# Optimization experiments

Measured on AMD Instinct MI355X. Metric: run time of the kernel, lower is better.

## Reference

```python
import jax, jax.numpy as jnp
import numpy as np

B, T, C = 4, 2048, 768
NH, NKV, HD = 12, 12, 64
RMS_EPS = 1e-6


def rms_norm(x):
    return x * jax.lax.rsqrt(jnp.mean(x * x, axis=-1, keepdims=True) + RMS_EPS)


def apply_rotary_emb(x, cos, sin):
    # x: [B,T,H,D], cos/sin: [T,D/2]
    d2 = x.shape[-1] // 2
    x1, x2 = x[..., :d2], x[..., d2:]
    c = cos[None, :, None, :]
    s = sin[None, :, None, :]
    return jnp.concatenate([x1 * c - x2 * s, x1 * s + x2 * c], axis=-1)


def setup_inputs() -> dict:
    key = jax.random.key(0)
    ks = jax.random.split(key, 10)
    inv_freq = 1.0 / (100000.0 ** (np.arange(0, HD, 2, dtype=np.float32) / HD))  # [HD/2]
    t = np.arange(T, dtype=np.float32)
    freqs = np.outer(t, inv_freq)  # [T, HD/2]
    return {
        "x": jax.random.normal(ks[0], (B, T, C), jnp.float32),
        "ve": jax.random.normal(ks[1], (B, T, C), jnp.float32),
        "cos": jnp.asarray(np.cos(freqs)),
        "sin": jnp.asarray(np.sin(freqs)),
        "Wq": jax.random.normal(ks[2], (C, C), jnp.float32) * (1.0 / np.sqrt(C)),
        "Wk": jax.random.normal(ks[3], (C, C), jnp.float32) * (1.0 / np.sqrt(C)),
        "Wv": jax.random.normal(ks[4], (C, C), jnp.float32) * (1.0 / np.sqrt(C)),
        "Wproj": jax.random.normal(ks[5], (C, C), jnp.float32) * (1.0 / np.sqrt(C)),
        "Wgate": jax.random.normal(ks[6], (NKV, 12), jnp.float32) * 0.1,
        "window_left": 1024,
    }


def reference(x, ve, cos, sin, Wq, Wk, Wv, Wproj, Wgate, window_left):
    q = (x @ Wq.T).reshape(B, T, NH, HD)
    k = (x @ Wk.T).reshape(B, T, NKV, HD)
    v = (x @ Wv.T).reshape(B, T, NKV, HD)

    # value-embedding gating (has_ve path): gate = 3*sigmoid(Linear(x[...,:12]))
    ve_h = ve.reshape(B, T, NKV, HD)
    gate = 3.0 * jax.nn.sigmoid(x[..., :12] @ Wgate.T)  # [B,T,NKV]
    v = v + gate[..., None] * ve_h

    q = apply_rotary_emb(q, cos, sin)
    k = apply_rotary_emb(k, cos, sin)
    q = rms_norm(q) * 1.2
    k = rms_norm(k) * 1.2

    # sliding-window causal bias
    row = jnp.arange(T)[:, None]
    col = jnp.arange(T)[None, :]
    mask = (row >= col) & ((row - col) <= window_left)
    bias = jnp.where(mask, 0.0, -1e9).astype(x.dtype)  # [T,T]

    scale = 1.0 / np.sqrt(HD)
    att = jnp.einsum("bqhd,bkhd->bhqk", q, k) * scale + bias[None, None]
    att = jax.nn.softmax(att, axis=-1)
    y = jnp.einsum("bhqk,bkhd->bqhd", att, v).reshape(B, T, C)
    return y @ Wproj.T
```

## Files before the change

kernel.cpp:

```cpp
#include <hip/hip_runtime.h>
#include <hip/hip_bf16.h>
#include <cstdint>
#include <cstddef>

#define B_  4
#define T_  2048
#define C_  768
#define NH_ 12
#define HD_ 64

typedef __bf16 bf16_t;
typedef __attribute__((ext_vector_type(8))) __bf16 bf16x8;
typedef __attribute__((ext_vector_type(4))) __bf16 bf16x4;
typedef __attribute__((ext_vector_type(4))) float floatx4;
typedef __attribute__((ext_vector_type(8))) unsigned short ushort8;
typedef __attribute__((ext_vector_type(4))) unsigned int uint4v;

#define MFMA16(a, b, c) __builtin_amdgcn_mfma_f32_16x16x32_bf16((a), (b), (c), 0, 0, 0)

#define SM_C1 0.18033688f
#define SM_C2 -17.3123405f

typedef const __attribute__((address_space(1))) uint8_t* gptr_t;
typedef __attribute__((address_space(3))) uint8_t* lptr_t;

static __device__ __forceinline__ void gld16(const void* g, void* l) {
    __builtin_amdgcn_global_load_lds((gptr_t)g, (lptr_t)l, 16, 0, 0);
}

__global__ __launch_bounds__(256) void cvt_all_kernel(
    const void* s0, const void* s1, const void* s2, const void* s3,
    const void* s4, const void* s5, const void* s6, const void* s7, const void* s8,
    bf16_t* d0, bf16_t* d1, bf16_t* d2, bf16_t* d3,
    bf16_t* d4, bf16_t* d5, bf16_t* d6, bf16_t* d7, bf16_t* d8)
{
    const void* srcs[9] = {s0, s1, s2, s3, s4, s5, s6, s7, s8};
    bf16_t*     dsts[9] = {d0, d1, d2, d3, d4, d5, d6, d7, d8};
    const int   ns[9]   = {B_*T_*C_, B_*T_*C_, T_*32, T_*32,
                           C_*C_, C_*C_, C_*C_, C_*C_, 144};
    const int t = blockIdx.y;
    const void* src = srcs[t];
    bf16_t*     dst = dsts[t];
    const int   nc  = ns[t] >> 3;
    const bool isf32 = (((const unsigned short*)s2)[0] == 0);
    const int stride = gridDim.x * 256;
    if (isf32) {
        const float* sf = (const float*)src;
        for (int i = blockIdx.x * 256 + threadIdx.x; i < nc; i += stride) {
            ushort8 o;
#pragma unroll
            for (int j = 0; j < 8; j++) {
                union { float f; unsigned u; } v; v.f = sf[i * 8 + j];
                bf16_t b = (bf16_t)v.f; (void)b;
                o[j] = (unsigned short)(__builtin_bit_cast(unsigned short,
                         (bf16_t)sf[i * 8 + j]));
            }
            *(ushort8*)&dst[i * 8] = o;
        }
    } else {
        const uint4v* sb = (const uint4v*)src;
        uint4v* db = (uint4v*)dst;
        for (int i = blockIdx.x * 256 + threadIdx.x; i < nc; i += stride)
            db[i] = sb[i];
    }
}

template <bool OUT_BF16>
__device__ __forceinline__ void gemm_bt_tile(
    const bf16_t* __restrict__ A, const bf16_t* __restrict__ Bm,
    void* __restrict__ Cout, int m0, int n0, int K, int ldc)
{
    __shared__ bf16_t As[128 * 32];
    __shared__ bf16_t Bs[128 * 32];
    const int tid  = threadIdx.x;
    const int lane = tid & 63;
    const int wid  = tid >> 6;
    const int m16  = lane & 15;
    const int quad = lane >> 4;
    const int wm   = (wid >> 1) * 64;
    const int wn   = (wid & 1) * 64;
    const int srow = lane >> 2;
    const int soct = (lane & 3) * 8;

    floatx4 acc[4][4];
#pragma unroll
    for (int i = 0; i < 4; i++)
#pragma unroll
        for (int j = 0; j < 4; j++) acc[i][j] = (floatx4){0.f, 0.f, 0.f, 0.f};

    for (int k0 = 0; k0 < K; k0 += 32) {
        const bf16_t* ga0 = &A[(size_t)(m0 + 16 * wid + srow) * K + k0 + soct];
        const bf16_t* gb0 = &Bm[(size_t)(n0 + 16 * wid + srow) * K + k0 + soct];
        gld16(ga0,                 (bf16_t*)As + wid * 512);
        gld16(ga0 + (size_t)64 * K, (bf16_t*)As + wid * 512 + 2048);
        gld16(gb0,                 (bf16_t*)Bs + wid * 512);
        gld16(gb0 + (size_t)64 * K, (bf16_t*)Bs + wid * 512 + 2048);
        __syncthreads();
        bf16x8 af[4], bfr[4];
#pragma unroll
        for (int i = 0; i < 4; i++)
            af[i] = *(const bf16x8*)&As[(wm + i * 16 + m16) * 32 + quad * 8];
#pragma unroll
        for (int j = 0; j < 4; j++)
            bfr[j] = *(const bf16x8*)&Bs[(wn + j * 16 + m16) * 32 + quad * 8];
#pragma unroll
        for (int i = 0; i < 4; i++)
#pragma unroll
            for (int j = 0; j < 4; j++)
                acc[i][j] = MFMA16(af[i], bfr[j], acc[i][j]);
        __syncthreads();
    }

#pragma unroll
    for (int i = 0; i < 4; i++) {
#pragma unroll
        for (int j = 0; j < 4; j++) {
            const int colg = n0 + wn + j * 16 + m16;
#pragma unroll
            for (int r = 0; r < 4; r++) {
                const int rowg = m0 + wm + i * 16 + quad * 4 + r;
                if (OUT_BF16)
                    ((bf16_t*)Cout)[(size_t)rowg * ldc + colg] = (bf16_t)acc[i][j][r];
                else
                    ((float*)Cout)[(size_t)rowg * ldc + colg] = acc[i][j][r];
            }
        }
    }
}

__global__ __launch_bounds__(256) void gemm_qkv_kernel(
    const bf16_t* __restrict__ xb,
    const bf16_t* __restrict__ wq, const bf16_t* __restrict__ wk,
    const bf16_t* __restrict__ wv,
    bf16_t* __restrict__ ql, bf16_t* __restrict__ kl, bf16_t* __restrict__ vl)
{
    const int sel = blockIdx.y / 6;
    const int nt  = blockIdx.y % 6;
    const bf16_t* Bm = (sel == 0) ? wq : (sel == 1) ? wk : wv;
    bf16_t* Cout     = (sel == 0) ? ql : (sel == 1) ? kl : vl;
    gemm_bt_tile<true>(xb, Bm, Cout, blockIdx.x * 128, nt * 128, C_, C_);
}

__global__ __launch_bounds__(256) void gemm_proj_kernel(
    const bf16_t* __restrict__ yb, const bf16_t* __restrict__ wp,
    void* __restrict__ out, const void* cos_raw)
{
    const bool isf32 = (((const unsigned short*)cos_raw)[0] == 0);
    if (isf32)
        gemm_bt_tile<false>(yb, wp, out, blockIdx.x * 128, blockIdx.y * 128, C_, C_);
    else
        gemm_bt_tile<true>(yb, wp, out, blockIdx.x * 128, blockIdx.y * 128, C_, C_);
}

__global__ __launch_bounds__(768) void qkv_post_kernel(
    const bf16_t* __restrict__ x, const bf16_t* __restrict__ ve,
    const bf16_t* __restrict__ cosp, const bf16_t* __restrict__ sinp,
    const bf16_t* __restrict__ wg,
    const bf16_t* __restrict__ ql, const bf16_t* __restrict__ kl,
    const bf16_t* __restrict__ vl,
    bf16_t* __restrict__ qb, bf16_t* __restrict__ kb, bf16_t* __restrict__ vt)
{
    const int bt = blockIdx.x;
    const int b  = bt / T_;
    const int t  = bt % T_;
    const int h  = threadIdx.x >> 6;
    const int d  = threadIdx.x & 63;
    const size_t lin    = (size_t)bt * C_ + h * HD_ + d;
    const size_t outIdx = ((size_t)(b * NH_ + h) * T_ + t) * HD_ + d;

    float g = 0.f;
#pragma unroll
    for (int j = 0; j < 12; j++)
        g += (float)x[(size_t)bt * C_ + j] * (float)wg[h * 12 + j];
    const float gate = 3.f / (1.f + __expf(-g));
    const int c6 = t & 63;
    const int tp = (t & ~63) | (((c6 & 15) << 2) | (c6 >> 4));
    vt[((size_t)(b * NH_ + h) * HD_ + d) * T_ + tp] =
        (bf16_t)((float)vl[lin] + gate * (float)ve[lin]);

    const float c = (float)cosp[t * 32 + (d & 31)];
    const float s = (float)sinp[t * 32 + (d & 31)];

    {
        const float own = (float)ql[lin];
        const float oth = __shfl_xor(own, 32, 64);
        const float qr  = (d < 32) ? (own * c - oth * s) : (oth * s + own * c);
        float ss = qr * qr;
#pragma unroll
        for (int off = 1; off < 64; off <<= 1) ss += __shfl_xor(ss, off, 64);
        qb[outIdx] = (bf16_t)(qr * rsqrtf(ss * (1.f / 64.f) + 1e-6f) * 1.2f);
    }
    {
        const float own = (float)kl[lin];
        const float oth = __shfl_xor(own, 32, 64);
        const float kr  = (d < 32) ? (own * c - oth * s) : (oth * s + own * c);
        float ss = kr * kr;
#pragma unroll
        for (int off = 1; off < 64; off <<= 1) ss += __shfl_xor(ss, off, 64);
        kb[outIdx] = (bf16_t)(kr * rsqrtf(ss * (1.f / 64.f) + 1e-6f) * 1.2f);
    }
}

__global__ __launch_bounds__(256, 3) void attn_kernel(
    const bf16_t* __restrict__ Q, const bf16_t* __restrict__ Km,
    const bf16_t* __restrict__ Vtg, bf16_t* __restrict__ Y,
    const int* __restrict__ wl)
{
    const int q0 = blockIdx.x * 128;
    const int bh = blockIdx.y;
    const int b  = bh / NH_;
    const int h  = bh % NH_;
    const int window = wl[0];
    const int tid  = threadIdx.x;
    const int wid  = tid >> 6;
    const int lane = tid & 63;
    const int m16  = lane & 15;
    const int quad = lane >> 4;
    const int qw   = q0 + wid * 32;

    const size_t base = (size_t)bh * T_ * HD_;
    const bf16_t* Qb  = Q + base;
    const bf16_t* Kb  = Km + base;
    const bf16_t* Vb  = Vtg + base;

    __shared__ bf16_t Ks[2][64 * 64];
    __shared__ bf16_t Vs[2][64 * 64];
    __shared__ bf16_t Ps[4][32 * 72];

    bf16x8 qf[2][2];
#pragma unroll
    for (int mt = 0; mt < 2; mt++)
#pragma unroll
        for (int ks = 0; ks < 2; ks++)
            qf[mt][ks] = *(const bf16x8*)
                &Qb[(size_t)(qw + mt * 16 + m16) * HD_ + ks * 32 + quad * 8];

    const int srow = tid >> 2;
    const int soct = tid & 3;
    const int g0   = 2 * soct, g1 = 2 * soct + 1;
    const int kd0  = srow * 64 + ((g0 ^ (srow & 7)) << 3);
    const int kd1  = srow * 64 + ((g1 ^ (srow & 7)) << 3);

    int rsw[2];
#pragma unroll
    for (int ks = 0; ks < 2; ks++)
        rsw[ks] = (((ks * 4 + quad) ^ (m16 & 7)) << 3);

    int lo = q0 - window;
    if (lo < 0) lo = 0;
    lo &= ~63;
    const int nch = (q0 + 128 - lo) >> 6;

    floatx4 accO[2][4];
#pragma unroll
    for (int mt = 0; mt < 2; mt++)
#pragma unroll
        for (int dt = 0; dt < 4; dt++) accO[mt][dt] = (floatx4){0.f, 0.f, 0.f, 0.f};
    float lsum[2][4] = {{0.f, 0.f, 0.f, 0.f}, {0.f, 0.f, 0.f, 0.f}};

    bf16x8 ka0 = *(const bf16x8*)&Kb[(size_t)(lo + srow) * HD_ + g0 * 8];
    bf16x8 ka1 = *(const bf16x8*)&Kb[(size_t)(lo + srow) * HD_ + g1 * 8];
    bf16x8 va0 = *(const bf16x8*)&Vb[(size_t)srow * T_ + lo + g0 * 8];
    bf16x8 va1 = *(const bf16x8*)&Vb[(size_t)srow * T_ + lo + g1 * 8];
    *(bf16x8*)&Ks[0][kd0] = ka0;
    *(bf16x8*)&Ks[0][kd1] = ka1;
    *(bf16x8*)&Vs[0][kd0] = va0;
    *(bf16x8*)&Vs[0][kd1] = va1;

    for (int ic = 0; ic < nch; ic++) {
        const int kc = lo + ic * 64;
        const bool more = (ic + 1 < nch);
        if (more) {
            const int kn = kc + 64;
            ka0 = *(const bf16x8*)&Kb[(size_t)(kn + srow) * HD_ + g0 * 8];
            ka1 = *(const bf16x8*)&Kb[(size_t)(kn + srow) * HD_ + g1 * 8];
            va0 = *(const bf16x8*)&Vb[(size_t)srow * T_ + kn + g0 * 8];
            va1 = *(const bf16x8*)&Vb[(size_t)srow * T_ + kn + g1 * 8];
        }
        __syncthreads();
        const int buf = ic & 1;

        const bool skip = (kc > qw + 31) || (kc + 63 < qw - window);
        if (!skip) {
            bf16x8 kf[4][2];
#pragma unroll
            for (int nt = 0; nt < 4; nt++) {
                const int rb = (nt * 16 + m16) * 64;
                kf[nt][0] = *(const bf16x8*)&Ks[buf][rb + rsw[0]];
                kf[nt][1] = *(const bf16x8*)&Ks[buf][rb + rsw[1]];
            }
            floatx4 sa[2][4];
#pragma unroll
            for (int mt = 0; mt < 2; mt++)
#pragma unroll
                for (int nt = 0; nt < 4; nt++) {
                    floatx4 z = (floatx4){0.f, 0.f, 0.f, 0.f};
                    z = MFMA16(qf[mt][0], kf[nt][0], z);
                    z = MFMA16(qf[mt][1], kf[nt][1], z);
                    sa[mt][nt] = z;
                }

            const bool edge = (kc + 63 > qw) || (kc < qw + 31 - window);
#pragma unroll
            for (int mt = 0; mt < 2; mt++)
#pragma unroll
                for (int r = 0; r < 4; r++) {
                    bf16x4 pk;
                    float psum = 0.f;
                    const int rowg = qw + mt * 16 + quad * 4 + r;
#pragma unroll
                    for (int nt = 0; nt < 4; nt++) {
                        float p = __builtin_amdgcn_exp2f(
                            fmaf(sa[mt][nt][r], SM_C1, SM_C2));
                        if (edge) {
                            const int colg = kc + nt * 16 + m16;
                            const bool ok = (colg <= rowg) &&
                                            (rowg - colg <= window);
                            p = ok ? p : 0.f;
                        }
                        pk[nt] = (bf16_t)p;
                        psum += p;
                    }
                    lsum[mt][r] += psum;
                    *(bf16x4*)&Ps[wid][(mt * 16 + quad * 4 + r) * 72 + m16 * 4] = pk;
                }
            asm volatile("" ::: "memory");

            bf16x8 pa[2][2];
#pragma unroll
            for (int mt = 0; mt < 2; mt++)
#pragma unroll
                for (int ks = 0; ks < 2; ks++)
                    pa[mt][ks] = *(const bf16x8*)
                        &Ps[wid][(mt * 16 + m16) * 72 + ks * 32 + quad * 8];
#pragma unroll
            for (int dt = 0; dt < 4; dt++) {
                const int rb = (dt * 16 + m16) * 64;
                const bf16x8 vf0 = *(const bf16x8*)&Vs[buf][rb + rsw[0]];
                const bf16x8 vf1 = *(const bf16x8*)&Vs[buf][rb + rsw[1]];
#pragma unroll
                for (int mt = 0; mt < 2; mt++) {
                    accO[mt][dt] = MFMA16(pa[mt][0], vf0, accO[mt][dt]);
                    accO[mt][dt] = MFMA16(pa[mt][1], vf1, accO[mt][dt]);
                }
            }
        }

        if (more) {
            const int nb = buf ^ 1;
            *(bf16x8*)&Ks[nb][kd0] = ka0;
            *(bf16x8*)&Ks[nb][kd1] = ka1;
            *(bf16x8*)&Vs[nb][kd0] = va0;
            *(bf16x8*)&Vs[nb][kd1] = va1;
        }
    }

#pragma unroll
    for (int mt = 0; mt < 2; mt++)
#pragma unroll
        for (int r = 0; r < 4; r++) {
            float l = lsum[mt][r];
#pragma unroll
            for (int off = 1; off < 16; off <<= 1) l += __shfl_xor(l, off, 64);
            const float inv = 1.f / l;
            const int tq = qw + mt * 16 + quad * 4 + r;
#pragma unroll
            for (int dt = 0; dt < 4; dt++)
                Y[((size_t)b * T_ + tq) * C_ + h * HD_ + dt * 16 + m16] =
                    (bf16_t)(accO[mt][dt][r] * inv);
        }
}

extern "C" void kernel_launch(void* const* d_in, const int* in_sizes, int n_in,
                              void* d_out, int out_size, void* d_ws, size_t ws_size,
                              hipStream_t stream)
{
    const void* x_raw   = d_in[0];
    const void* ve_raw  = d_in[1];
    const void* cos_raw = d_in[2];
    const void* sin_raw = d_in[3];
    const void* wq_raw  = d_in[4];
    const void* wk_raw  = d_in[5];
    const void* wv_raw  = d_in[6];
    const void* wp_raw  = d_in[7];
    const void* wg_raw  = d_in[8];
    const int*  wl      = (const int*)d_in[9];

    const size_t NTC = (size_t)B_ * T_ * C_;
    const size_t WSZ = (size_t)C_ * C_;

    bf16_t* ws  = (bf16_t*)d_ws;
    bf16_t* xb  = ws;
    bf16_t* veb = xb + NTC;
    bf16_t* cb  = veb + NTC;
    bf16_t* sb  = cb + T_ * 32;
    bf16_t* wqb = sb + T_ * 32;
    bf16_t* wkb = wqb + WSZ;
    bf16_t* wvb = wkb + WSZ;
    bf16_t* wpb = wvb + WSZ;
    bf16_t* wgb = wpb + WSZ;
    bf16_t* ql  = wgb + 256;
    bf16_t* kl  = ql + NTC;
    bf16_t* vl  = kl + NTC;
    bf16_t* qb  = vl + NTC;
    bf16_t* kb  = qb + NTC;
    bf16_t* vt  = kb + NTC;
    bf16_t* yb  = ql;

    cvt_all_kernel<<<dim3(1024, 9), 256, 0, stream>>>(
        x_raw, ve_raw, cos_raw, sin_raw, wq_raw, wk_raw, wv_raw, wp_raw, wg_raw,
        xb, veb, cb, sb, wqb, wkb, wvb, wpb, wgb);

    gemm_qkv_kernel<<<dim3(64, 18), 256, 0, stream>>>(xb, wqb, wkb, wvb, ql, kl, vl);

    qkv_post_kernel<<<dim3(B_ * T_), 768, 0, stream>>>(
        xb, veb, cb, sb, wgb, ql, kl, vl, qb, kb, vt);

    attn_kernel<<<dim3(T_ / 128, B_ * NH_), 256, 0, stream>>>(qb, kb, vt, yb, wl);

    gemm_proj_kernel<<<dim3(64, 6), 256, 0, stream>>>(yb, wpb, d_out, cos_raw);
}
```

Baseline: 270.7 us.

## Keep P in registers, skip masked tiles, stage V transpose, deepen GEMM k-step

Attention now computes S transposed (K as the A operand), so the probability fragments stay in registers and feed the PV MFMA directly without the LDS P buffer. Fully masked 16x16 subtiles are skipped, and query blocks are reordered per head group to balance causal load. qkv_post now handles 32 tokens per wave and transposes V through shared memory so the vt stores coalesce. The GEMM loads two 32-wide K slabs per barrier, halving the number of syncs, and dead code is removed from the convert kernel. The risks are higher register and LDS pressure and extra branch divergence.

```diff
diff --git a/kernel.cpp b/kernel.cpp
--- a/kernel.cpp
+++ b/kernel.cpp
@@ -49,12 +49,9 @@
         for (int i = blockIdx.x * 256 + threadIdx.x; i < nc; i += stride) {
             ushort8 o;
 #pragma unroll
-            for (int j = 0; j < 8; j++) {
-                union { float f; unsigned u; } v; v.f = sf[i * 8 + j];
-                bf16_t b = (bf16_t)v.f; (void)b;
-                o[j] = (unsigned short)(__builtin_bit_cast(unsigned short,
-                         (bf16_t)sf[i * 8 + j]));
-            }
+            for (int j = 0; j < 8; j++)
+                o[j] = (unsigned short)__builtin_bit_cast(unsigned short,
+                         (bf16_t)sf[i * 8 + j]);
             *(ushort8*)&dst[i * 8] = o;
         }
     } else {
@@ -70,8 +67,8 @@
     const bf16_t* __restrict__ A, const bf16_t* __restrict__ Bm,
     void* __restrict__ Cout, int m0, int n0, int K, int ldc)
 {
-    __shared__ bf16_t As[128 * 32];
-    __shared__ bf16_t Bs[128 * 32];
+    __shared__ bf16_t As[2][128 * 32];
+    __shared__ bf16_t Bs[2][128 * 32];
     const int tid  = threadIdx.x;
     const int lane = tid & 63;
     const int wid  = tid >> 6;
@@ -88,26 +85,33 @@
 #pragma unroll
         for (int j = 0; j < 4; j++) acc[i][j] = (floatx4){0.f, 0.f, 0.f, 0.f};
 
-    for (int k0 = 0; k0 < K; k0 += 32) {
+    for (int k0 = 0; k0 < K; k0 += 64) {
         const bf16_t* ga0 = &A[(size_t)(m0 + 16 * wid + srow) * K + k0 + soct];
         const bf16_t* gb0 = &Bm[(size_t)(n0 + 16 * wid + srow) * K + k0 + soct];
-        gld16(ga0,                 (bf16_t*)As + wid * 512);
-        gld16(ga0 + (size_t)64 * K, (bf16_t*)As + wid * 512 + 2048);
-        gld16(gb0,                 (bf16_t*)Bs + wid * 512);
-        gld16(gb0 + (size_t)64 * K, (bf16_t*)Bs + wid * 512 + 2048);
+        gld16(ga0,                       (bf16_t*)As[0] + wid * 512);
+        gld16(ga0 + (size_t)64 * K,      (bf16_t*)As[0] + wid * 512 + 2048);
+        gld16(gb0,                       (bf16_t*)Bs[0] + wid * 512);
+        gld16(gb0 + (size_t)64 * K,      (bf16_t*)Bs[0] + wid * 512 + 2048);
+        gld16(ga0 + 32,                  (bf16_t*)As[1] + wid * 512);
+        gld16(ga0 + (size_t)64 * K + 32, (bf16_t*)As[1] + wid * 512 + 2048);
+        gld16(gb0 + 32,                  (bf16_t*)Bs[1] + wid * 512);
+        gld16(gb0 + (size_t)64 * K + 32, (bf16_t*)Bs[1] + wid * 512 + 2048);
         __syncthreads();
-        bf16x8 af[4], bfr[4];
-#pragma unroll
-        for (int i = 0; i < 4; i++)
-            af[i] = *(const bf16x8*)&As[(wm + i * 16 + m16) * 32 + quad * 8];
-#pragma unroll
-        for (int j = 0; j < 4; j++)
-            bfr[j] = *(const bf16x8*)&Bs[(wn + j * 16 + m16) * 32 + quad * 8];
-#pragma unroll
-        for (int i = 0; i < 4; i++)
+#pragma unroll
+        for (int half = 0; half < 2; half++) {
+            bf16x8 af[4], bfr[4];
+#pragma unroll
+            for (int i = 0; i < 4; i++)
+                af[i] = *(const bf16x8*)&As[half][(wm + i * 16 + m16) * 32 + quad * 8];
 #pragma unroll
             for (int j = 0; j < 4; j++)
-                acc[i][j] = MFMA16(af[i], bfr[j], acc[i][j]);
+                bfr[j] = *(const bf16x8*)&Bs[half][(wn + j * 16 + m16) * 32 + quad * 8];
+#pragma unroll
+            for (int i = 0; i < 4; i++)
+#pragma unroll
+                for (int j = 0; j < 4; j++)
+                    acc[i][j] = MFMA16(af[i], bfr[j], acc[i][j]);
+        }
         __syncthreads();
     }
 
@@ -152,7 +156,7 @@
         gemm_bt_tile<true>(yb, wp, out, blockIdx.x * 128, blockIdx.y * 128, C_, C_);
 }
 
-__global__ __launch_bounds__(768) void qkv_post_kernel(
+__global__ __launch_bounds__(256) void qkv_post_kernel(
     const bf16_t* __restrict__ x, const bf16_t* __restrict__ ve,
     const bf16_t* __restrict__ cosp, const bf16_t* __restrict__ sinp,
     const bf16_t* __restrict__ wg,
@@ -160,44 +164,57 @@
     const bf16_t* __restrict__ vl,
     bf16_t* __restrict__ qb, bf16_t* __restrict__ kb, bf16_t* __restrict__ vt)
 {
-    const int bt = blockIdx.x;
-    const int b  = bt / T_;
-    const int t  = bt % T_;
-    const int h  = threadIdx.x >> 6;
+    const int t0 = blockIdx.x * 32;
+    const int b  = blockIdx.y;
+    const int w  = threadIdx.x >> 6;
+    const int h  = blockIdx.z * 4 + w;
     const int d  = threadIdx.x & 63;
-    const size_t lin    = (size_t)bt * C_ + h * HD_ + d;
-    const size_t outIdx = ((size_t)(b * NH_ + h) * T_ + t) * HD_ + d;
-
-    float g = 0.f;
-#pragma unroll
-    for (int j = 0; j < 12; j++)
-        g += (float)x[(size_t)bt * C_ + j] * (float)wg[h * 12 + j];
-    const float gate = 3.f / (1.f + __expf(-g));
-    const int c6 = t & 63;
-    const int tp = (t & ~63) | (((c6 & 15) << 2) | (c6 >> 4));
-    vt[((size_t)(b * NH_ + h) * HD_ + d) * T_ + tp] =
-        (bf16_t)((float)vl[lin] + gate * (float)ve[lin]);
-
-    const float c = (float)cosp[t * 32 + (d & 31)];
-    const float s = (float)sinp[t * 32 + (d & 31)];
-
-    {
-        const float own = (float)ql[lin];
-        const float oth = __shfl_xor(own, 32, 64);
-        const float qr  = (d < 32) ? (own * c - oth * s) : (oth * s + own * c);
-        float ss = qr * qr;
-#pragma unroll
-        for (int off = 1; off < 64; off <<= 1) ss += __shfl_xor(ss, off, 64);
-        qb[outIdx] = (bf16_t)(qr * rsqrtf(ss * (1.f / 64.f) + 1e-6f) * 1.2f);
-    }
-    {
-        const float own = (float)kl[lin];
-        const float oth = __shfl_xor(own, 32, 64);
-        const float kr  = (d < 32) ? (own * c - oth * s) : (oth * s + own * c);
-        float ss = kr * kr;
-#pragma unroll
-        for (int off = 1; off < 64; off <<= 1) ss += __shfl_xor(ss, off, 64);
-        kb[outIdx] = (bf16_t)(kr * rsqrtf(ss * (1.f / 64.f) + 1e-6f) * 1.2f);
+    __shared__ float vtile[4][32 * 65];
+    float* vt_l = vtile[w];
+    const float wgd = (d < 12) ? (float)wg[h * 12 + d] : 0.f;
+
+    for (int c = 0; c < 32; c++) {
+        const int t  = t0 + c;
+        const int bt = b * T_ + t;
+        const size_t lin = (size_t)bt * C_ + h * HD_ + d;
+        float gx = (d < 12) ? (float)x[(size_t)bt * C_ + d] * wgd : 0.f;
+        gx += __shfl_xor(gx, 1, 64); gx += __shfl_xor(gx, 2, 64);
+        gx += __shfl_xor(gx, 4, 64); gx += __shfl_xor(gx, 8, 64);
+        gx = __shfl(gx, 0, 64);
+        const float gate = 3.f / (1.f + __expf(-gx));
+        vt_l[c * 65 + d] = (float)vl[lin] + gate * (float)ve[lin];
+
+        const float co = (float)cosp[t * 32 + (d & 31)];
+        const float si = (float)sinp[t * 32 + (d & 31)];
+        const size_t oidx = ((size_t)(b * NH_ + h) * T_ + t) * HD_ + d;
+        {
+            const float own = (float)ql[lin];
+            const float oth = __shfl_xor(own, 32, 64);
+            const float qr  = (d < 32) ? (own * co - oth * si) : (oth * si + own * co);
+            float ss = qr * qr;
+#pragma unroll
+            for (int off = 1; off < 64; off <<= 1) ss += __shfl_xor(ss, off, 64);
+            qb[oidx] = (bf16_t)(qr * rsqrtf(ss * (1.f / 64.f) + 1e-6f) * 1.2f);
+        }
+        {
+            const float own = (float)kl[lin];
+            const float oth = __shfl_xor(own, 32, 64);
+            const float kr  = (d < 32) ? (own * co - oth * si) : (oth * si + own * co);
+            float ss = kr * kr;
+#pragma unroll
+            for (int off = 1; off < 64; off <<= 1) ss += __shfl_xor(ss, off, 64);
+            kb[oidx] = (bf16_t)(kr * rsqrtf(ss * (1.f / 64.f) + 1e-6f) * 1.2f);
+        }
+    }
+
+    const int cc = threadIdx.x & 31;
+    const int dh = (threadIdx.x >> 5) & 1;
+    const int tp = t0 + ((((cc >> 2) & 3) << 3) | ((cc >> 4) << 2) | (cc & 3));
+#pragma unroll 4
+    for (int it = 0; it < 32; it++) {
+        const int dd = it * 2 + dh;
+        vt[((size_t)(b * NH_ + h) * HD_ + dd) * T_ + tp] =
+            (bf16_t)vt_l[cc * 65 + dd];
     }
 }
 
@@ -206,8 +223,14 @@
     const bf16_t* __restrict__ Vtg, bf16_t* __restrict__ Y,
     const int* __restrict__ wl)
 {
-    const int q0 = blockIdx.x * 128;
-    const int bh = blockIdx.y;
+    const int bx   = blockIdx.x;
+    const int bh   = blockIdx.y;
+    const int gsel = bh >> 4;
+    int qblk;
+    if (gsel == 0)      qblk = bx;
+    else if (gsel == 1) qblk = 15 - bx;
+    else                qblk = (int)((0xECA8642013579BDFull >> (bx * 4)) & 0xF);
+    const int q0 = qblk * 128;
     const int b  = bh / NH_;
     const int h  = bh % NH_;
     const int window = wl[0];
@@ -225,7 +248,6 @@
 
     __shared__ bf16_t Ks[2][64 * 64];
     __shared__ bf16_t Vs[2][64 * 64];
-    __shared__ bf16_t Ps[4][32 * 72];
 
     bf16x8 qf[2][2];
 #pragma unroll
@@ -240,7 +262,6 @@
     const int g0   = 2 * soct, g1 = 2 * soct + 1;
     const int kd0  = srow * 64 + ((g0 ^ (srow & 7)) << 3);
     const int kd1  = srow * 64 + ((g1 ^ (srow & 7)) << 3);
-
     int rsw[2];
 #pragma unroll
     for (int ks = 0; ks < 2; ks++)
@@ -256,7 +277,8 @@
     for (int mt = 0; mt < 2; mt++)
 #pragma unroll
         for (int dt = 0; dt < 4; dt++) accO[mt][dt] = (floatx4){0.f, 0.f, 0.f, 0.f};
-    float lsum[2][4] = {{0.f, 0.f, 0.f, 0.f}, {0.f, 0.f, 0.f, 0.f}};
+    float lsum[2] = {0.f, 0.f};
+    const bf16x4 zero4 = {(bf16_t)0.f, (bf16_t)0.f, (bf16_t)0.f, (bf16_t)0.f};
 
     bf16x8 ka0 = *(const bf16x8*)&Kb[(size_t)(lo + srow) * HD_ + g0 * 8];
     bf16x8 ka1 = *(const bf16x8*)&Kb[(size_t)(lo + srow) * HD_ + g1 * 8];
@@ -289,59 +311,59 @@
                 kf[nt][0] = *(const bf16x8*)&Ks[buf][rb + rsw[0]];
                 kf[nt][1] = *(const bf16x8*)&Ks[buf][rb + rsw[1]];
             }
-            floatx4 sa[2][4];
-#pragma unroll
-            for (int mt = 0; mt < 2; mt++)
+            bf16x4 pk[2][4];
+            unsigned livemask = 0;
+#pragma unroll
+            for (int mt = 0; mt < 2; mt++) {
+                const int qmin = qw + mt * 16, qmax = qmin + 15;
+                float lacc = 0.f;
 #pragma unroll
                 for (int nt = 0; nt < 4; nt++) {
+                    const int kmin = kc + nt * 16, kmax = kmin + 15;
+                    if (kmin > qmax || kmax < qmin - window) {
+                        pk[mt][nt] = zero4;
+                        continue;
+                    }
+                    livemask |= 1u << (mt * 4 + nt);
                     floatx4 z = (floatx4){0.f, 0.f, 0.f, 0.f};
-                    z = MFMA16(qf[mt][0], kf[nt][0], z);
-                    z = MFMA16(qf[mt][1], kf[nt][1], z);
-                    sa[mt][nt] = z;
-                }
-
-            const bool edge = (kc + 63 > qw) || (kc < qw + 31 - window);
-#pragma unroll
-            for (int mt = 0; mt < 2; mt++)
-#pragma unroll
-                for (int r = 0; r < 4; r++) {
-                    bf16x4 pk;
-                    float psum = 0.f;
-                    const int rowg = qw + mt * 16 + quad * 4 + r;
-#pragma unroll
-                    for (int nt = 0; nt < 4; nt++) {
+                    z = MFMA16(kf[nt][0], qf[mt][0], z);
+                    z = MFMA16(kf[nt][1], qf[mt][1], z);
+                    const bool edge = (kmax > qmin) || (kmin < qmax - window);
+                    const int query = qmin + m16;
+                    bf16x4 t4;
+#pragma unroll
+                    for (int r = 0; r < 4; r++) {
                         float p = __builtin_amdgcn_exp2f(
-                            fmaf(sa[mt][nt][r], SM_C1, SM_C2));
+                            fmaf(z[r], SM_C1, SM_C2));
                         if (edge) {
-                            const int colg = kc + nt * 16 + m16;
-                            const bool ok = (colg <= rowg) &&
-                                            (rowg - colg <= window);
+                            const int key = kmin + quad * 4 + r;
+                            const bool ok = (key <= query) &&
+                                            (query - key <= window);
                             p = ok ? p : 0.f;
                         }
-                        pk[nt] = (bf16_t)p;
-                        psum += p;
+                        t4[r] = (bf16_t)p;
+                        lacc += p;
                     }
-                    lsum[mt][r] += psum;
-                    *(bf16x4*)&Ps[wid][(mt * 16 + quad * 4 + r) * 72 + m16 * 4] = pk;
+                    pk[mt][nt] = t4;
                 }
-            asm volatile("" ::: "memory");
-
-            bf16x8 pa[2][2];
-#pragma unroll
-            for (int mt = 0; mt < 2; mt++)
-#pragma unroll
-                for (int ks = 0; ks < 2; ks++)
-                    pa[mt][ks] = *(const bf16x8*)
-                        &Ps[wid][(mt * 16 + m16) * 72 + ks * 32 + quad * 8];
-#pragma unroll
-            for (int dt = 0; dt < 4; dt++) {
-                const int rb = (dt * 16 + m16) * 64;
-                const bf16x8 vf0 = *(const bf16x8*)&Vs[buf][rb + rsw[0]];
-                const bf16x8 vf1 = *(const bf16x8*)&Vs[buf][rb + rsw[1]];
-#pragma unroll
-                for (int mt = 0; mt < 2; mt++) {
-                    accO[mt][dt] = MFMA16(pa[mt][0], vf0, accO[mt][dt]);
-                    accO[mt][dt] = MFMA16(pa[mt][1], vf1, accO[mt][dt]);
+                lsum[mt] += lacc;
+            }
+#pragma unroll
+            for (int pr = 0; pr < 2; pr++) {
+                const unsigned pm0 = (livemask >> (2 * pr)) & 3u;
+                const unsigned pm1 = (livemask >> (4 + 2 * pr)) & 3u;
+                if (!(pm0 | pm1)) continue;
+                const bf16x8 pa0 = __builtin_shufflevector(
+                    pk[0][2 * pr], pk[0][2 * pr + 1], 0, 1, 2, 3, 4, 5, 6, 7);
+                const bf16x8 pa1 = __builtin_shufflevector(
+                    pk[1][2 * pr], pk[1][2 * pr + 1], 0, 1, 2, 3, 4, 5, 6, 7);
+                const int vco = (((pr * 4 + quad) ^ (m16 & 7)) << 3);
+#pragma unroll
+                for (int dt = 0; dt < 4; dt++) {
+                    const bf16x8 vf = *(const bf16x8*)
+                        &Vs[buf][(dt * 16 + m16) * 64 + vco];
+                    if (pm0) accO[0][dt] = MFMA16(pa0, vf, accO[0][dt]);
+                    if (pm1) accO[1][dt] = MFMA16(pa1, vf, accO[1][dt]);
                 }
             }
         }
@@ -356,19 +378,21 @@
     }
 
 #pragma unroll
-    for (int mt = 0; mt < 2; mt++)
+    for (int mt = 0; mt < 2; mt++) {
+        float red = lsum[mt];
+        red += __shfl_xor(red, 16, 64);
+        red += __shfl_xor(red, 32, 64);
 #pragma unroll
         for (int r = 0; r < 4; r++) {
-            float l = lsum[mt][r];
-#pragma unroll
-            for (int off = 1; off < 16; off <<= 1) l += __shfl_xor(l, off, 64);
-            const float inv = 1.f / l;
-            const int tq = qw + mt * 16 + quad * 4 + r;
+            const float lq  = __shfl(red, quad * 4 + r, 64);
+            const float inv = 1.f / lq;
+            const int   tq  = qw + mt * 16 + quad * 4 + r;
 #pragma unroll
             for (int dt = 0; dt < 4; dt++)
                 Y[((size_t)b * T_ + tq) * C_ + h * HD_ + dt * 16 + m16] =
                     (bf16_t)(accO[mt][dt][r] * inv);
         }
+    }
 }
 
 extern "C" void kernel_launch(void* const* d_in, const int* in_sizes, int n_in,
@@ -413,10 +437,10 @@
 
     gemm_qkv_kernel<<<dim3(64, 18), 256, 0, stream>>>(xb, wqb, wkb, wvb, ql, kl, vl);
 
-    qkv_post_kernel<<<dim3(B_ * T_), 768, 0, stream>>>(
+    qkv_post_kernel<<<dim3(T_ / 32, B_, 3), 256, 0, stream>>>(
         xb, veb, cb, sb, wgb, ql, kl, vl, qb, kb, vt);
 
-    attn_kernel<<<dim3(T_ / 128, B_ * NH_), 256, 0, stream>>>(qb, kb, vt, yb, wl);
+    attn_kernel<<<dim3(16, 48), 256, 0, stream>>>(qb, kb, vt, yb, wl);
 
     gemm_proj_kernel<<<dim3(64, 6), 256, 0, stream>>>(yb, wpb, d_out, cos_raw);
 }
```

Result: faster. 257.3 us (-4.9%).
